# Kernel optimization log

Hardware: AMD Instinct MI355X
Metric: run time of the kernel (lower is better)

The kernel has to match this reference:

```python
import jax, jax.numpy as jnp
import numpy as np

H = 128  # LSTM hidden size


def lstm_layer(x, Wih, Whh, bih, bhh):
    # x: [B, T, Fin]; Wih: [4H, Fin]; Whh: [4H, H]; biases: [4H]
    xg = jnp.einsum('btf,gf->btg', x, Wih) + bih  # precompute input gates [B,T,4H]
    B = x.shape[0]
    h0 = jnp.zeros((B, H), x.dtype)
    c0 = jnp.zeros((B, H), x.dtype)

    def step(carry, xt):
        h, c = carry
        g = xt + h @ Whh.T + bhh  # [B,4H]
        i, f, gg, o = jnp.split(g, 4, axis=-1)  # torch gate order: i,f,g,o
        i = jax.nn.sigmoid(i)
        f = jax.nn.sigmoid(f)
        gg = jnp.tanh(gg)
        o = jax.nn.sigmoid(o)
        c = f * c + i * gg
        h = o * jnp.tanh(c)
        return (h, c), h

    (hT, cT), hs = jax.lax.scan(step, (h0, c0), jnp.swapaxes(xg, 0, 1))
    return jnp.swapaxes(hs, 0, 1), hT  # all-step outputs [B,T,H], final h [B,H]


def setup_inputs() -> dict:
    key = jax.random.key(0)
    ks = jax.random.split(key, 20)
    B, T, F = 512, 912, 32
    s = 1.0 / np.sqrt(H)  # torch LSTM/Linear init scale
    u = lambda k, shape: jax.random.uniform(k, shape, jnp.float32, -s, s)
    return {
        'x': jax.random.normal(ks[0], (B, T, F), jnp.float32),
        'Wih0': u(ks[1], (4 * H, F)),
        'Whh0': u(ks[2], (4 * H, H)),
        'bih0': u(ks[3], (4 * H,)),
        'bhh0': u(ks[4], (4 * H,)),
        'Wih123': u(ks[5], (3, 4 * H, H)),
        'Whh123': u(ks[6], (3, 4 * H, H)),
        'bih123': u(ks[7], (3, 4 * H)),
        'bhh123': u(ks[8], (3, 4 * H)),
        'Wopt': u(ks[9], (4, H)), 'bopt': u(ks[10], (4,)),
        'Wlot': u(ks[11], (4, H)), 'blot': u(ks[12], (4,)),
        'Wtp': u(ks[13], (4, H)), 'btp': u(ks[14], (4,)),
        'Wsl': u(ks[15], (4, H)), 'bsl': u(ks[16], (4,)),
    }


def reference(x, Wih0, Whh0, bih0, bhh0, Wih123, Whh123, bih123, bhh123,
              Wopt, bopt, Wlot, blot, Wtp, btp, Wsl, bsl):
    out, h0f = lstm_layer(x, Wih0, Whh0, bih0, bhh0)
    finals = [h0f]
    for l in range(3):  # fixed small layer loop
        out, hf = lstm_layer(out, Wih123[l], Whh123[l], bih123[l], bhh123[l])
        finals.append(hf)
    hN = jnp.stack(finals)  # h_n: [4, B, H] (final hidden per layer, as torch returns)
    # heads: Sequential applies softmax/sigmoid once, forward applies it again
    opt = jax.nn.softmax(jax.nn.softmax(hN @ Wopt.T + bopt, axis=-1), axis=-1)
    lot = jax.nn.sigmoid(jax.nn.sigmoid(hN @ Wlot.T + blot))
    tp = jax.nn.sigmoid(jax.nn.sigmoid(hN @ Wtp.T + btp))
    sl = jax.nn.sigmoid(jax.nn.sigmoid(hN @ Wsl.T + bsl))
    return (opt, tp, sl, lot)
```

## Files before the change

kernel.cpp:

```cpp
#include <hip/hip_runtime.h>

#define DEV __device__ __forceinline__

typedef __attribute__((ext_vector_type(8))) short short8;
typedef __attribute__((ext_vector_type(4))) float floatx4;
typedef unsigned long long ull;

static constexpr int B_ = 512, T_ = 912, H_ = 128, F_ = 32;
static constexpr size_t HN_OFF   = 1024;
static constexpr size_t XT_OFF   = HN_OFF + (size_t)4 * 512 * 128 * 2;
static constexpr size_t RING_OFF = XT_OFF + (size_t)T_ * B_ * F_ * 2;
static constexpr size_t RING_BPG = 8 * 32768;

template <int N> struct IC { static constexpr int value = N; };

DEV unsigned short bf16rne(float f) {
    unsigned u = __builtin_bit_cast(unsigned, f);
    u += 0x7FFFu + ((u >> 16) & 1u);
    return (unsigned short)(u >> 16);
}
DEV float bf16tof(unsigned short u) {
    return __builtin_bit_cast(float, ((unsigned)u) << 16);
}
DEV float fastsig(float y) {
    return __builtin_amdgcn_rcpf(1.f + __builtin_amdgcn_exp2f(y));
}
DEV float sigm(float x) { return fastsig(-1.44269504f * x); }
DEV unsigned ald(const unsigned* p) {
    return __hip_atomic_load(p, __ATOMIC_RELAXED, __HIP_MEMORY_SCOPE_AGENT);
}
DEV void ast32(unsigned* p, unsigned v) {
    __hip_atomic_store(p, v, __ATOMIC_RELAXED, __HIP_MEMORY_SCOPE_AGENT);
}
DEV ull ald8(const ull* p) {
    return __hip_atomic_load(p, __ATOMIC_RELAXED, __HIP_MEMORY_SCOPE_AGENT);
}
DEV void ast8(ull* p, ull v) {
    __hip_atomic_store(p, v, __ATOMIC_RELAXED, __HIP_MEMORY_SCOPE_AGENT);
}
DEV void bar_fast() {
    asm volatile("s_waitcnt lgkmcnt(0)\n\ts_barrier" ::: "memory");
}

__global__ __launch_bounds__(256) void xpose(const float* __restrict__ x,
                                             unsigned short* __restrict__ xT) {
    int tid = blockIdx.x * 256 + threadIdx.x;
    if (tid >= B_ * T_ * 4) return;
    int k = tid & 3;
    int r = tid >> 2;
    int b = r / T_;
    int t = r - b * T_;
    const float* p = x + ((size_t)r * 32 + k * 8);
    short8 v;
#pragma unroll
    for (int j = 0; j < 8; j++) v[j] = (short)bf16rne(p[j]);
    *(short8*)(xT + ((size_t)t * 512 + b) * 32 + k * 8) = v;
}

__global__ __launch_bounds__(512, 2) void lstm_scan(
    const float* __restrict__ Wih0, const float* __restrict__ Whh0,
    const float* __restrict__ bih0, const float* __restrict__ bhh0,
    const float* __restrict__ Wih123, const float* __restrict__ Whh123,
    const float* __restrict__ bih123, const float* __restrict__ bhh123,
    char* __restrict__ ws) {
    const int tid  = threadIdx.x;
    const int wv   = tid >> 6;
    const int lane = tid & 63;
    const int col  = lane & 15;
    const int quad = lane >> 4;
    const int layer = blockIdx.x >> 5;
    const int grp   = blockIdx.x & 31;
    const int b0    = grp * 16;

    unsigned* flags = (unsigned*)ws;
    unsigned* cons  = (unsigned*)(ws + 512);
    char* hN8 = ws + HN_OFF;
    const char* xTB = ws + XT_OFF;

    __shared__ unsigned short Ah[16][16][132];
    __shared__ unsigned short Xl[16][16][132];
    char* AhB = (char*)Ah;
    char* XlB = (char*)Xl;

    for (int i = tid; i < 16 * 16 * 132; i += 512) {
        ((unsigned short*)Ah)[i] = 0;
        ((unsigned short*)Xl)[i] = 0;
    }

    short8 wh[4][4];
    short8 wx[4][4];
    float  bias_q[4];
    {
        const float *Wih, *Whh, *bih, *bhh;
        int kin, KX;
        if (layer == 0) { Wih = Wih0; Whh = Whh0; bih = bih0; bhh = bhh0; kin = 32; KX = 1; }
        else {
            Wih = Wih123 + (size_t)(layer - 1) * 512 * 128;
            Whh = Whh123 + (size_t)(layer - 1) * 512 * 128;
            bih = bih123 + (size_t)(layer - 1) * 512;
            bhh = bhh123 + (size_t)(layer - 1) * 512;
            kin = 128; KX = 4;
        }
#pragma unroll
        for (int q = 0; q < 4; q++) {
            const float sc = (q == 2) ? -2.88539008f : -1.44269504f;
            int row = q * 128 + wv * 16 + col;
            bias_q[q] = (bih[row] + bhh[row]) * sc;
#pragma unroll
            for (int kt = 0; kt < 4; kt++) {
                const float* ph = Whh + (size_t)row * 128 + kt * 32 + quad * 8;
                short8 v;
#pragma unroll
                for (int j = 0; j < 8; j++) v[j] = (short)bf16rne(ph[j] * sc);
                wh[q][kt] = v;
            }
#pragma unroll
            for (int kt = 0; kt < 4; kt++) {
                short8 v = {0, 0, 0, 0, 0, 0, 0, 0};
                if (kt < KX) {
                    const float* px = Wih + (size_t)row * kin + kt * 32 + quad * 8;
#pragma unroll
                    for (int j = 0; j < 8; j++) v[j] = (short)bf16rne(px[j] * sc);
                }
                wx[q][kt] = v;
            }
        }
    }

    unsigned* myflag   = &flags[layer * 32 + grp];
    unsigned* prevflag = &flags[(layer > 0 ? layer - 1 : 0) * 32 + grp];
    unsigned* mycons   = &cons[(layer > 0 ? layer - 1 : 0) * 32 + grp];
    unsigned* nextcons = &cons[layer * 32 + grp];
    char* prodRing = ws + RING_OFF + (size_t)(layer * 32 + grp) * RING_BPG;
    char* consRing = ws + RING_OFF + (size_t)((layer > 0 ? layer - 1 : 0) * 32 + grp) * RING_BPG;

    const int ahrd  = col * 264 + quad * 16;
    const int hwr   = (quad * 4) * 264 + (wv * 16 + col) * 2;
    const int exOff = (tid >> 5) * 264 + (tid & 31) * 8;
    const int consOff = (tid >> 5) * 256 + (tid & 31) * 8;
    const int xgOff = (tid >> 6) * 32768 + b0 * 64 + (tid & 63) * 16;
    const int xlw0  = (tid >> 6) * 4224 + ((tid >> 2) & 15) * 264 + (tid & 3) * 16;

    ull    xin[8];
    short8 xv = {0, 0, 0, 0, 0, 0, 0, 0};
    unsigned pf = 0, pc = 0;
    float c4[4] = {0.f, 0.f, 0.f, 0.f};
    floatx4 accx[4];

    __syncthreads();

    if (layer > 0) {
        if (tid == 0) { while (ald(prevflag) < 2u) {} }
        __syncthreads();
#pragma unroll
        for (int j = 0; j < 16; j++) {
            ull d = ald8((const ull*)(consRing + (size_t)j * 4096 + consOff));
            *(ull*)(XlB + exOff + j * 4224) = d;
        }
    } else {
#pragma unroll
        for (int c0 = 0; c0 < 2; c0++) {
            short8 v = *(const short8*)(xTB + (size_t)c0 * 262144 + xgOff);
            *(short8*)(XlB + xlw0 + c0 * 33792) = v;
        }
    }
    __syncthreads();

    {
        short8 ax0[4];
#pragma unroll
        for (int kt = 0; kt < 4; kt++)
            ax0[kt] = *(const short8*)(XlB + ahrd + 0 * 4224 + kt * 64);
#pragma unroll
        for (int q = 0; q < 4; q++) {
            floatx4 a = {bias_q[q], bias_q[q], bias_q[q], bias_q[q]};
            accx[q] = a;
        }
#pragma unroll
        for (int kt = 0; kt < 4; kt++)
#pragma unroll
            for (int q = 0; q < 4; q++)
                accx[q] = __builtin_amdgcn_mfma_f32_16x16x32_bf16(ax0[kt], wx[q][kt], accx[q], 0, 0, 0);
    }

    int c = 0;
    auto step = [&](auto UC) {
        constexpr int u   = UC.value;
        constexpr bool bnd = (u == 0 || u == 8);
        constexpr bool stg = (u == 3 || u == 11);
        constexpr bool ver = (u == 7 || u == 15);
        constexpr int sph = (u < 8) ? 8 : 0;
        const int cc = c + (u >> 3);
        if (bnd) {
            if (tid == 0) {
                if (layer > 0 && cc <= 111) pf = ald(prevflag);
                if (layer < 3 && cc >= 8)   pc = ald(nextcons);
            }
            if (layer < 3 && cc >= 1) {
                char* rb = prodRing + (size_t)((cc - 1) & 7) * 32768 + tid * 8;
#pragma unroll
                for (int p = 0; p < 8; p++) {
                    ull hv = *(const ull*)(AhB + exOff + (sph + p) * 4224);
                    ast8((ull*)(rb + p * 4096), hv);
                }
            }
            if (layer > 0 && cc <= 112) {
                const char* rb2 = consRing + (size_t)((cc + 1) & 7) * 32768 + consOff;
#pragma unroll
                for (int j = 0; j < 8; j++)
                    xin[j] = ald8((const ull*)(rb2 + j * 4096));
            }
            if (layer == 0 && cc <= 112)
                xv = *(const short8*)(xTB + (size_t)(cc + 1) * 262144 + xgOff);
        }
        if (stg) {
            if (layer > 0) {
#pragma unroll
                for (int j = 0; j < 8; j++)
                    *(ull*)(XlB + exOff + (sph + j) * 4224) = xin[j];
            } else {
                *(short8*)(XlB + xlw0 + sph * 4224) = xv;
            }
        }
        short8 ah[4], axn[4];
#pragma unroll
        for (int kt = 0; kt < 4; kt++) {
            ah[kt]  = *(const short8*)(AhB + ahrd + ((u + 15) & 15) * 4224 + kt * 64);
            axn[kt] = *(const short8*)(XlB + ahrd + ((u + 1) & 15) * 4224 + kt * 64);
        }
        floatx4 acc[4];
#pragma unroll
        for (int q = 0; q < 4; q++) acc[q] = accx[q];
#pragma unroll
        for (int kt = 0; kt < 4; kt++)
#pragma unroll
            for (int q = 0; q < 4; q++)
                acc[q] = __builtin_amdgcn_mfma_f32_16x16x32_bf16(ah[kt], wh[q][kt], acc[q], 0, 0, 0);
#pragma unroll
        for (int q = 0; q < 4; q++) {
            floatx4 a = {bias_q[q], bias_q[q], bias_q[q], bias_q[q]};
            accx[q] = a;
        }
#pragma unroll
        for (int r = 0; r < 4; r++) {
            float iv = fastsig(acc[0][r]);
            float fv = fastsig(acc[1][r]);
            float gr = fastsig(acc[2][r]);
            float ov = fastsig(acc[3][r]);
#pragma unroll
            for (int q = 0; q < 4; q++)
                accx[q] = __builtin_amdgcn_mfma_f32_16x16x32_bf16(axn[r], wx[q][r], accx[q], 0, 0, 0);
            float gt = 2.f * gr - 1.f;
            float cv = fv * c4[r] + iv * gt;
            c4[r] = cv;
            float rc = fastsig(-2.88539008f * cv);
            float hv = ov * (2.f * rc - 1.f);
            *(unsigned short*)(AhB + hwr + u * 4224 + r * 264) = bf16rne(hv);
        }
        if (stg) {
            __syncthreads();
            if (tid == 0) {
                if (layer < 3 && cc >= 1) ast32(myflag, (unsigned)cc);
                if (layer > 0) ast32(mycons, (unsigned)(cc + 2));
            }
        } else {
            if (ver && tid == 0) {
                if (layer > 0 && cc <= 111) {
                    unsigned tgt = cc + 3;
                    if (pf < tgt) while (ald(prevflag) < tgt) {}
                }
                if (layer < 3 && cc >= 8) {
                    unsigned tgt = cc - 7;
                    if (pc < tgt) while (ald(nextcons) < tgt) {}
                }
            }
            bar_fast();
        }
    };

    for (c = 0; c < 114; c += 2) {
        step(IC<0>{});  step(IC<1>{});  step(IC<2>{});  step(IC<3>{});
        step(IC<4>{});  step(IC<5>{});  step(IC<6>{});  step(IC<7>{});
        step(IC<8>{});  step(IC<9>{});  step(IC<10>{}); step(IC<11>{});
        step(IC<12>{}); step(IC<13>{}); step(IC<14>{}); step(IC<15>{});
    }

    if (layer < 3) {
        char* rb = prodRing + (size_t)(113 & 7) * 32768 + tid * 8;
#pragma unroll
        for (int p = 0; p < 8; p++) {
            ull hv = *(const ull*)(AhB + exOff + (8 + p) * 4224);
            ast8((ull*)(rb + p * 4096), hv);
        }
    }
    __syncthreads();
    if (tid == 0 && layer < 3) ast32(myflag, 114u);
    {
        ull hv = *(const ull*)(AhB + exOff + 15 * 4224);
        *(ull*)(hN8 + ((size_t)layer * 512 + b0 + (tid >> 5)) * 256 + (tid & 31) * 8) = hv;
    }
}

__global__ __launch_bounds__(256) void heads(
    const unsigned short* __restrict__ hN,
    const float* __restrict__ Wopt, const float* __restrict__ bopt,
    const float* __restrict__ Wlot, const float* __restrict__ blot,
    const float* __restrict__ Wtp,  const float* __restrict__ btp,
    const float* __restrict__ Wsl,  const float* __restrict__ bsl,
    float* __restrict__ out) {
    int tid = blockIdx.x * 256 + threadIdx.x;
    if (tid >= 4 * 4 * 512) return;
    int b  = tid & 511;
    int l  = (tid >> 9) & 3;
    int hd = tid >> 11;
    const float *W, *bb;
    if      (hd == 0) { W = Wopt; bb = bopt; }
    else if (hd == 1) { W = Wtp;  bb = btp;  }
    else if (hd == 2) { W = Wsl;  bb = bsl;  }
    else              { W = Wlot; bb = blot; }
    const unsigned short* h = hN + ((size_t)l * 512 + b) * 128;
    float z0 = bb[0], z1 = bb[1], z2 = bb[2], z3 = bb[3];
    for (int i = 0; i < 128; i++) {
        float hv = bf16tof(h[i]);
        z0 += hv * W[0 * 128 + i];
        z1 += hv * W[1 * 128 + i];
        z2 += hv * W[2 * 128 + i];
        z3 += hv * W[3 * 128 + i];
    }
    float o0, o1, o2, o3;
    if (hd == 0) {
        float m = fmaxf(fmaxf(z0, z1), fmaxf(z2, z3));
        float e0 = __builtin_amdgcn_exp2f((z0 - m) * 1.44269504f);
        float e1 = __builtin_amdgcn_exp2f((z1 - m) * 1.44269504f);
        float e2 = __builtin_amdgcn_exp2f((z2 - m) * 1.44269504f);
        float e3 = __builtin_amdgcn_exp2f((z3 - m) * 1.44269504f);
        float rs = __builtin_amdgcn_rcpf(e0 + e1 + e2 + e3);
        float p0 = e0 * rs, p1 = e1 * rs, p2 = e2 * rs, p3 = e3 * rs;
        float m2 = fmaxf(fmaxf(p0, p1), fmaxf(p2, p3));
        float f0 = __builtin_amdgcn_exp2f((p0 - m2) * 1.44269504f);
        float f1 = __builtin_amdgcn_exp2f((p1 - m2) * 1.44269504f);
        float f2 = __builtin_amdgcn_exp2f((p2 - m2) * 1.44269504f);
        float f3 = __builtin_amdgcn_exp2f((p3 - m2) * 1.44269504f);
        float rs2 = __builtin_amdgcn_rcpf(f0 + f1 + f2 + f3);
        o0 = f0 * rs2; o1 = f1 * rs2; o2 = f2 * rs2; o3 = f3 * rs2;
    } else {
        o0 = sigm(sigm(z0)); o1 = sigm(sigm(z1));
        o2 = sigm(sigm(z2)); o3 = sigm(sigm(z3));
    }
    float* o = out + (size_t)hd * 8192 + ((size_t)l * 512 + b) * 4;
    o[0] = o0; o[1] = o1; o[2] = o2; o[3] = o3;
}

extern "C" void kernel_launch(void* const* d_in, const int* in_sizes, int n_in,
                              void* d_out, int out_size, void* d_ws, size_t ws_size,
                              hipStream_t stream) {
    (void)in_sizes; (void)n_in; (void)out_size; (void)ws_size;
    const float* x      = (const float*)d_in[0];
    const float* Wih0   = (const float*)d_in[1];
    const float* Whh0   = (const float*)d_in[2];
    const float* bih0   = (const float*)d_in[3];
    const float* bhh0   = (const float*)d_in[4];
    const float* Wih123 = (const float*)d_in[5];
    const float* Whh123 = (const float*)d_in[6];
    const float* bih123 = (const float*)d_in[7];
    const float* bhh123 = (const float*)d_in[8];
    const float* Wopt = (const float*)d_in[9];
    const float* bopt = (const float*)d_in[10];
    const float* Wlot = (const float*)d_in[11];
    const float* blot = (const float*)d_in[12];
    const float* Wtp  = (const float*)d_in[13];
    const float* btp  = (const float*)d_in[14];
    const float* Wsl  = (const float*)d_in[15];
    const float* bsl  = (const float*)d_in[16];
    char* ws = (char*)d_ws;

    hipMemsetAsync(ws, 0, 1024, stream);
    xpose<<<(B_ * T_ * 4 + 255) / 256, 256, 0, stream>>>(x, (unsigned short*)(ws + XT_OFF));
    lstm_scan<<<128, 512, 0, stream>>>(Wih0, Whh0, bih0, bhh0,
                                       Wih123, Whh123, bih123, bhh123, ws);
    heads<<<32, 256, 0, stream>>>((const unsigned short*)(ws + HN_OFF),
                                  Wopt, bopt, Wlot, blot, Wtp, btp, Wsl, bsl,
                                  (float*)d_out);
}
```

Measured before the change: 2.123 ms.

## Process 32 batch rows per block and feed input operands from registers

Each workgroup now handles 32 batch rows instead of 16, which halves the grid to 64 blocks and doubles the ring slot size. Every weight fragment held in registers is reused across two MFMA row tiles. The LDS staging buffer for inputs is removed: the next step's input fragments are loaded straight from the ring or the transposed x into registers, with the input-gate MFMAs issued each step before the recurrent ones. The aim is to amortise the per-step barrier and synchronisation cost over more work and to cut LDS traffic. The cost is a longer serial critical path per step and higher register pressure. The consumer acknowledgement offset also changes from cc+2 to cc.

```diff
diff --git a/kernel.cpp b/kernel.cpp
--- a/kernel.cpp
+++ b/kernel.cpp
@@ -5,12 +5,13 @@
 typedef __attribute__((ext_vector_type(8))) short short8;
 typedef __attribute__((ext_vector_type(4))) float floatx4;
 typedef unsigned long long ull;
+typedef __attribute__((ext_vector_type(2))) unsigned long long ull2;
 
 static constexpr int B_ = 512, T_ = 912, H_ = 128, F_ = 32;
 static constexpr size_t HN_OFF   = 1024;
 static constexpr size_t XT_OFF   = HN_OFF + (size_t)4 * 512 * 128 * 2;
 static constexpr size_t RING_OFF = XT_OFF + (size_t)T_ * B_ * F_ * 2;
-static constexpr size_t RING_BPG = 8 * 32768;
+static constexpr size_t RING_BPG = 8 * 65536;
 
 template <int N> struct IC { static constexpr int value = N; };
 
@@ -37,6 +38,12 @@
 }
 DEV void ast8(ull* p, ull v) {
     __hip_atomic_store(p, v, __ATOMIC_RELAXED, __HIP_MEMORY_SCOPE_AGENT);
+}
+DEV short8 ld_ring16(const char* p) {
+    ull2 r;
+    r.x = ald8((const ull*)p);
+    r.y = ald8((const ull*)(p + 8));
+    return __builtin_bit_cast(short8, r);
 }
 DEV void bar_fast() {
     asm volatile("s_waitcnt lgkmcnt(0)\n\ts_barrier" ::: "memory");
@@ -68,24 +75,20 @@
     const int lane = tid & 63;
     const int col  = lane & 15;
     const int quad = lane >> 4;
-    const int layer = blockIdx.x >> 5;
-    const int grp   = blockIdx.x & 31;
-    const int b0    = grp * 16;
+    const int layer = blockIdx.x >> 4;
+    const int grp   = blockIdx.x & 15;
+    const int b0    = grp * 32;
+    const bool lay0 = (layer == 0);
 
     unsigned* flags = (unsigned*)ws;
     unsigned* cons  = (unsigned*)(ws + 512);
     char* hN8 = ws + HN_OFF;
     const char* xTB = ws + XT_OFF;
 
-    __shared__ unsigned short Ah[16][16][132];
-    __shared__ unsigned short Xl[16][16][132];
+    __shared__ unsigned short Ah[16][32][132];
     char* AhB = (char*)Ah;
-    char* XlB = (char*)Xl;
-
-    for (int i = tid; i < 16 * 16 * 132; i += 512) {
-        ((unsigned short*)Ah)[i] = 0;
-        ((unsigned short*)Xl)[i] = 0;
-    }
+
+    for (int i = tid; i < 16 * 32 * 132; i += 512) ((unsigned short*)Ah)[i] = 0;
 
     short8 wh[4][4];
     short8 wx[4][4];
@@ -127,60 +130,42 @@
         }
     }
 
-    unsigned* myflag   = &flags[layer * 32 + grp];
-    unsigned* prevflag = &flags[(layer > 0 ? layer - 1 : 0) * 32 + grp];
-    unsigned* mycons   = &cons[(layer > 0 ? layer - 1 : 0) * 32 + grp];
-    unsigned* nextcons = &cons[layer * 32 + grp];
-    char* prodRing = ws + RING_OFF + (size_t)(layer * 32 + grp) * RING_BPG;
-    char* consRing = ws + RING_OFF + (size_t)((layer > 0 ? layer - 1 : 0) * 32 + grp) * RING_BPG;
+    unsigned* myflag   = &flags[layer * 16 + grp];
+    unsigned* prevflag = &flags[(layer > 0 ? layer - 1 : 0) * 16 + grp];
+    unsigned* mycons   = &cons[(layer > 0 ? layer - 1 : 0) * 16 + grp];
+    unsigned* nextcons = &cons[layer * 16 + grp];
+    char* prodRing = ws + RING_OFF + (size_t)(layer * 16 + grp) * RING_BPG;
+    char* consRing = ws + RING_OFF + (size_t)((layer > 0 ? layer - 1 : 0) * 16 + grp) * RING_BPG;
 
     const int ahrd  = col * 264 + quad * 16;
     const int hwr   = (quad * 4) * 264 + (wv * 16 + col) * 2;
-    const int exOff = (tid >> 5) * 264 + (tid & 31) * 8;
-    const int consOff = (tid >> 5) * 256 + (tid & 31) * 8;
-    const int xgOff = (tid >> 6) * 32768 + b0 * 64 + (tid & 63) * 16;
-    const int xlw0  = (tid >> 6) * 4224 + ((tid >> 2) & 15) * 264 + (tid & 3) * 16;
-
-    ull    xin[8];
-    short8 xv = {0, 0, 0, 0, 0, 0, 0, 0};
+    const int exRow = tid >> 4;
+    const int exB   = (tid & 15) * 16;
+    const int xroff = col * 256 + quad * 16;
+    const int xoff0 = (b0 + col) * 64 + quad * 16;
+
+    const short8 z8 = {0, 0, 0, 0, 0, 0, 0, 0};
+    short8 xb0[4], xb1[4];
+#pragma unroll
+    for (int kt = 0; kt < 4; kt++) { xb0[kt] = z8; xb1[kt] = z8; }
     unsigned pf = 0, pc = 0;
-    float c4[4] = {0.f, 0.f, 0.f, 0.f};
-    floatx4 accx[4];
+    float c8[8] = {0.f, 0.f, 0.f, 0.f, 0.f, 0.f, 0.f, 0.f};
 
     __syncthreads();
 
-    if (layer > 0) {
+    if (!lay0) {
         if (tid == 0) { while (ald(prevflag) < 2u) {} }
         __syncthreads();
-#pragma unroll
-        for (int j = 0; j < 16; j++) {
-            ull d = ald8((const ull*)(consRing + (size_t)j * 4096 + consOff));
-            *(ull*)(XlB + exOff + j * 4224) = d;
+        const char* rb0 = consRing + xroff;
+#pragma unroll
+        for (int kt = 0; kt < 4; kt++) {
+            xb0[kt] = ld_ring16(rb0 + kt * 64);
+            xb1[kt] = ld_ring16(rb0 + 4096 + kt * 64);
         }
     } else {
-#pragma unroll
-        for (int c0 = 0; c0 < 2; c0++) {
-            short8 v = *(const short8*)(xTB + (size_t)c0 * 262144 + xgOff);
-            *(short8*)(XlB + xlw0 + c0 * 33792) = v;
-        }
-    }
-    __syncthreads();
-
-    {
-        short8 ax0[4];
-#pragma unroll
-        for (int kt = 0; kt < 4; kt++)
-            ax0[kt] = *(const short8*)(XlB + ahrd + 0 * 4224 + kt * 64);
-#pragma unroll
-        for (int q = 0; q < 4; q++) {
-            floatx4 a = {bias_q[q], bias_q[q], bias_q[q], bias_q[q]};
-            accx[q] = a;
-        }
-#pragma unroll
-        for (int kt = 0; kt < 4; kt++)
-#pragma unroll
-            for (int q = 0; q < 4; q++)
-                accx[q] = __builtin_amdgcn_mfma_f32_16x16x32_bf16(ax0[kt], wx[q][kt], accx[q], 0, 0, 0);
+        const char* px = xTB + xoff0;
+        xb0[0] = *(const short8*)px;
+        xb1[0] = *(const short8*)(px + 1024);
     }
 
     int c = 0;
@@ -191,77 +176,104 @@
         constexpr bool ver = (u == 7 || u == 15);
         constexpr int sph = (u < 8) ? 8 : 0;
         const int cc = c + (u >> 3);
+        const int t  = cc * 8 + (u & 7);
+
         if (bnd) {
             if (tid == 0) {
                 if (layer > 0 && cc <= 111) pf = ald(prevflag);
                 if (layer < 3 && cc >= 8)   pc = ald(nextcons);
             }
             if (layer < 3 && cc >= 1) {
-                char* rb = prodRing + (size_t)((cc - 1) & 7) * 32768 + tid * 8;
+                char* rb = prodRing + (size_t)((cc - 1) & 7) * 65536 + exRow * 256 + exB;
+                const char* src = AhB + sph * 8448 + exRow * 264 + exB;
 #pragma unroll
                 for (int p = 0; p < 8; p++) {
-                    ull hv = *(const ull*)(AhB + exOff + (sph + p) * 4224);
-                    ast8((ull*)(rb + p * 4096), hv);
-                }
-            }
-            if (layer > 0 && cc <= 112) {
-                const char* rb2 = consRing + (size_t)((cc + 1) & 7) * 32768 + consOff;
-#pragma unroll
-                for (int j = 0; j < 8; j++)
-                    xin[j] = ald8((const ull*)(rb2 + j * 4096));
-            }
-            if (layer == 0 && cc <= 112)
-                xv = *(const short8*)(xTB + (size_t)(cc + 1) * 262144 + xgOff);
-        }
-        if (stg) {
-            if (layer > 0) {
-#pragma unroll
-                for (int j = 0; j < 8; j++)
-                    *(ull*)(XlB + exOff + (sph + j) * 4224) = xin[j];
-            } else {
-                *(short8*)(XlB + xlw0 + sph * 4224) = xv;
-            }
-        }
-        short8 ah[4], axn[4];
+                    ull h0 = *(const ull*)(src + p * 8448);
+                    ull h1 = *(const ull*)(src + p * 8448 + 8);
+                    ast8((ull*)(rb + p * 8192), h0);
+                    ast8((ull*)(rb + p * 8192 + 8), h1);
+                }
+            }
+        }
+
+        const int slR = (u + 15) & 15;
+        short8 ah0[4], ah1[4];
+        const char* ab = AhB + slR * 8448 + ahrd;
 #pragma unroll
         for (int kt = 0; kt < 4; kt++) {
-            ah[kt]  = *(const short8*)(AhB + ahrd + ((u + 15) & 15) * 4224 + kt * 64);
-            axn[kt] = *(const short8*)(XlB + ahrd + ((u + 1) & 15) * 4224 + kt * 64);
-        }
-        floatx4 acc[4];
-#pragma unroll
-        for (int q = 0; q < 4; q++) acc[q] = accx[q];
-#pragma unroll
-        for (int kt = 0; kt < 4; kt++)
-#pragma unroll
-            for (int q = 0; q < 4; q++)
-                acc[q] = __builtin_amdgcn_mfma_f32_16x16x32_bf16(ah[kt], wh[q][kt], acc[q], 0, 0, 0);
+            ah0[kt] = *(const short8*)(ab + kt * 64);
+            ah1[kt] = *(const short8*)(ab + 4224 + kt * 64);
+        }
+
+        floatx4 acc[4][2];
 #pragma unroll
         for (int q = 0; q < 4; q++) {
             floatx4 a = {bias_q[q], bias_q[q], bias_q[q], bias_q[q]};
-            accx[q] = a;
-        }
-#pragma unroll
-        for (int r = 0; r < 4; r++) {
-            float iv = fastsig(acc[0][r]);
-            float fv = fastsig(acc[1][r]);
-            float gr = fastsig(acc[2][r]);
-            float ov = fastsig(acc[3][r]);
-#pragma unroll
-            for (int q = 0; q < 4; q++)
-                accx[q] = __builtin_amdgcn_mfma_f32_16x16x32_bf16(axn[r], wx[q][r], accx[q], 0, 0, 0);
-            float gt = 2.f * gr - 1.f;
-            float cv = fv * c4[r] + iv * gt;
-            c4[r] = cv;
-            float rc = fastsig(-2.88539008f * cv);
-            float hv = ov * (2.f * rc - 1.f);
-            *(unsigned short*)(AhB + hwr + u * 4224 + r * 264) = bf16rne(hv);
-        }
+            acc[q][0] = a; acc[q][1] = a;
+        }
+        if (lay0) {
+#pragma unroll
+            for (int q = 0; q < 4; q++) {
+                acc[q][0] = __builtin_amdgcn_mfma_f32_16x16x32_bf16(xb0[0], wx[q][0], acc[q][0], 0, 0, 0);
+                acc[q][1] = __builtin_amdgcn_mfma_f32_16x16x32_bf16(xb1[0], wx[q][0], acc[q][1], 0, 0, 0);
+            }
+        } else {
+#pragma unroll
+            for (int kt = 0; kt < 4; kt++)
+#pragma unroll
+                for (int q = 0; q < 4; q++) {
+                    acc[q][0] = __builtin_amdgcn_mfma_f32_16x16x32_bf16(xb0[kt], wx[q][kt], acc[q][0], 0, 0, 0);
+                    acc[q][1] = __builtin_amdgcn_mfma_f32_16x16x32_bf16(xb1[kt], wx[q][kt], acc[q][1], 0, 0, 0);
+                }
+        }
+
+        if (t < 911) {
+            if (lay0) {
+                const char* px = xTB + (size_t)(t + 1) * 32768 + xoff0;
+                xb0[0] = *(const short8*)px;
+                xb1[0] = *(const short8*)(px + 1024);
+            } else {
+                const char* rb2 = consRing + (size_t)(((t + 1) >> 3) & 7) * 65536
+                                  + (size_t)((t + 1) & 7) * 8192 + xroff;
+#pragma unroll
+                for (int kt = 0; kt < 4; kt++) {
+                    xb0[kt] = ld_ring16(rb2 + kt * 64);
+                    xb1[kt] = ld_ring16(rb2 + 4096 + kt * 64);
+                }
+            }
+        }
+
+#pragma unroll
+        for (int kt = 0; kt < 4; kt++)
+#pragma unroll
+            for (int q = 0; q < 4; q++) {
+                acc[q][0] = __builtin_amdgcn_mfma_f32_16x16x32_bf16(ah0[kt], wh[q][kt], acc[q][0], 0, 0, 0);
+                acc[q][1] = __builtin_amdgcn_mfma_f32_16x16x32_bf16(ah1[kt], wh[q][kt], acc[q][1], 0, 0, 0);
+            }
+
+        char* hb = AhB + (u & 15) * 8448 + hwr;
+#pragma unroll
+        for (int rt = 0; rt < 2; rt++)
+#pragma unroll
+            for (int r = 0; r < 4; r++) {
+                float iv = fastsig(acc[0][rt][r]);
+                float fv = fastsig(acc[1][rt][r]);
+                float gr = fastsig(acc[2][rt][r]);
+                float ov = fastsig(acc[3][rt][r]);
+                float gt = 2.f * gr - 1.f;
+                const int ci = rt * 4 + r;
+                float cv = fv * c8[ci] + iv * gt;
+                c8[ci] = cv;
+                float rc = fastsig(-2.88539008f * cv);
+                float hv = ov * (2.f * rc - 1.f);
+                *(unsigned short*)(hb + rt * 4224 + r * 264) = bf16rne(hv);
+            }
+
         if (stg) {
             __syncthreads();
             if (tid == 0) {
                 if (layer < 3 && cc >= 1) ast32(myflag, (unsigned)cc);
-                if (layer > 0) ast32(mycons, (unsigned)(cc + 2));
+                if (layer > 0) ast32(mycons, (unsigned)cc);
             }
         } else {
             if (ver && tid == 0) {
@@ -286,18 +298,25 @@
     }
 
     if (layer < 3) {
-        char* rb = prodRing + (size_t)(113 & 7) * 32768 + tid * 8;
+        char* rb = prodRing + (size_t)(113 & 7) * 65536 + exRow * 256 + exB;
+        const char* src = AhB + 8 * 8448 + exRow * 264 + exB;
 #pragma unroll
         for (int p = 0; p < 8; p++) {
-            ull hv = *(const ull*)(AhB + exOff + (8 + p) * 4224);
-            ast8((ull*)(rb + p * 4096), hv);
+            ull h0 = *(const ull*)(src + p * 8448);
+            ull h1 = *(const ull*)(src + p * 8448 + 8);
+            ast8((ull*)(rb + p * 8192), h0);
+            ast8((ull*)(rb + p * 8192 + 8), h1);
         }
     }
     __syncthreads();
     if (tid == 0 && layer < 3) ast32(myflag, 114u);
     {
-        ull hv = *(const ull*)(AhB + exOff + 15 * 4224);
-        *(ull*)(hN8 + ((size_t)layer * 512 + b0 + (tid >> 5)) * 256 + (tid & 31) * 8) = hv;
+        const char* src = AhB + 15 * 8448 + exRow * 264 + exB;
+        ull h0 = *(const ull*)src;
+        ull h1 = *(const ull*)(src + 8);
+        char* dst = hN8 + ((size_t)layer * 512 + b0 + exRow) * 256 + exB;
+        *(ull*)dst = h0;
+        *(ull*)(dst + 8) = h1;
     }
 }
 
@@ -376,8 +395,8 @@
 
     hipMemsetAsync(ws, 0, 1024, stream);
     xpose<<<(B_ * T_ * 4 + 255) / 256, 256, 0, stream>>>(x, (unsigned short*)(ws + XT_OFF));
-    lstm_scan<<<128, 512, 0, stream>>>(Wih0, Whh0, bih0, bhh0,
-                                       Wih123, Whh123, bih123, bhh123, ws);
+    lstm_scan<<<64, 512, 0, stream>>>(Wih0, Whh0, bih0, bhh0,
+                                      Wih123, Whh123, bih123, bhh123, ws);
     heads<<<32, 256, 0, stream>>>((const unsigned short*)(ws + HN_OFF),
                                   Wopt, bopt, Wlot, blot, Wtp, btp, Wsl, bsl,
                                   (float*)d_out);
```

After: 5.116 ms. 2.41x slower.

## Process two 16-row batch groups per block to halve scan grid

Applied to the files above, without the earlier changes.

Each block now handles two independent 16-sequence groups (A and B), interleaving their recurrent MFMA chains, so the grid shrinks from 128 to 64 blocks. The input projection is computed inline each step (layer 0 reads x directly from global memory) instead of being pipelined one step ahead. The ring exchange is reworked into per-step slot stores and loads with an 8-step chunk. The aim is to hide MFMA and transcendental latency through two independent dependency chains per wave, and to cut the number of cross-block flag handoffs. The cost is twice the per-step work on each block's critical path, the input-GEMM latency now sitting on that path, and fewer CUs in use.

```diff
diff --git a/kernel.cpp b/kernel.cpp
--- a/kernel.cpp
+++ b/kernel.cpp
@@ -68,23 +68,28 @@
     const int lane = tid & 63;
     const int col  = lane & 15;
     const int quad = lane >> 4;
-    const int layer = blockIdx.x >> 5;
-    const int grp   = blockIdx.x & 31;
-    const int b0    = grp * 16;
+    const int layer = blockIdx.x >> 4;
+    const int g     = blockIdx.x & 15;
+    const int b0    = g * 32;
+    const bool lay0 = (layer == 0);
 
     unsigned* flags = (unsigned*)ws;
     unsigned* cons  = (unsigned*)(ws + 512);
     char* hN8 = ws + HN_OFF;
     const char* xTB = ws + XT_OFF;
 
-    __shared__ unsigned short Ah[16][16][132];
-    __shared__ unsigned short Xl[16][16][132];
-    char* AhB = (char*)Ah;
-    char* XlB = (char*)Xl;
-
-    for (int i = tid; i < 16 * 16 * 132; i += 512) {
-        ((unsigned short*)Ah)[i] = 0;
-        ((unsigned short*)Xl)[i] = 0;
+    __shared__ unsigned short AhA[8][16][132];
+    __shared__ unsigned short AhB[8][16][132];
+    __shared__ unsigned short XlA[8][16][132];
+    __shared__ unsigned short XlB[8][16][132];
+    char* AhAB = (char*)AhA;
+    char* AhBB = (char*)AhB;
+    char* XlAB = (char*)XlA;
+    char* XlBB = (char*)XlB;
+
+    for (int i = tid; i < 8 * 16 * 132; i += 512) {
+        ((unsigned short*)AhA)[i] = 0; ((unsigned short*)AhB)[i] = 0;
+        ((unsigned short*)XlA)[i] = 0; ((unsigned short*)XlB)[i] = 0;
     }
 
     short8 wh[4][4];
@@ -127,150 +132,192 @@
         }
     }
 
-    unsigned* myflag   = &flags[layer * 32 + grp];
-    unsigned* prevflag = &flags[(layer > 0 ? layer - 1 : 0) * 32 + grp];
-    unsigned* mycons   = &cons[(layer > 0 ? layer - 1 : 0) * 32 + grp];
-    unsigned* nextcons = &cons[layer * 32 + grp];
-    char* prodRing = ws + RING_OFF + (size_t)(layer * 32 + grp) * RING_BPG;
-    char* consRing = ws + RING_OFF + (size_t)((layer > 0 ? layer - 1 : 0) * 32 + grp) * RING_BPG;
+    unsigned* myflag   = &flags[layer * 16 + g];
+    unsigned* prevflag = &flags[(layer > 0 ? layer - 1 : 0) * 16 + g];
+    unsigned* mycons   = &cons[(layer > 0 ? layer - 1 : 0) * 16 + g];
+    unsigned* nextcons = &cons[layer * 16 + g];
+    char* prodA = ws + RING_OFF + (size_t)(layer * 32 + 2 * g) * RING_BPG;
+    char* prodB = prodA + RING_BPG;
+    char* consAp = ws + RING_OFF + (size_t)((layer > 0 ? layer - 1 : 0) * 32 + 2 * g) * RING_BPG;
+    char* consBp = consAp + RING_BPG;
 
     const int ahrd  = col * 264 + quad * 16;
     const int hwr   = (quad * 4) * 264 + (wv * 16 + col) * 2;
-    const int exOff = (tid >> 5) * 264 + (tid & 31) * 8;
-    const int consOff = (tid >> 5) * 256 + (tid & 31) * 8;
-    const int xgOff = (tid >> 6) * 32768 + b0 * 64 + (tid & 63) * 16;
-    const int xlw0  = (tid >> 6) * 4224 + ((tid >> 2) & 15) * 264 + (tid & 3) * 16;
-
-    ull    xin[8];
-    short8 xv = {0, 0, 0, 0, 0, 0, 0, 0};
+    const int exA   = (tid >> 5) * 264 + (tid & 31) * 8;
+    const int rgo   = tid << 3;
+    const int xoffA = (b0 + col) * 64 + quad * 16;
+
+    ull xrA[2] = {0, 0}, xrB[2] = {0, 0};
     unsigned pf = 0, pc = 0;
-    float c4[4] = {0.f, 0.f, 0.f, 0.f};
-    floatx4 accx[4];
+    float c4A[4] = {0.f, 0.f, 0.f, 0.f};
+    float c4B[4] = {0.f, 0.f, 0.f, 0.f};
 
     __syncthreads();
 
-    if (layer > 0) {
+    if (!lay0) {
         if (tid == 0) { while (ald(prevflag) < 2u) {} }
         __syncthreads();
 #pragma unroll
-        for (int j = 0; j < 16; j++) {
-            ull d = ald8((const ull*)(consRing + (size_t)j * 4096 + consOff));
-            *(ull*)(XlB + exOff + j * 4224) = d;
-        }
-    } else {
-#pragma unroll
-        for (int c0 = 0; c0 < 2; c0++) {
-            short8 v = *(const short8*)(xTB + (size_t)c0 * 262144 + xgOff);
-            *(short8*)(XlB + xlw0 + c0 * 33792) = v;
-        }
-    }
-    __syncthreads();
-
-    {
-        short8 ax0[4];
-#pragma unroll
-        for (int kt = 0; kt < 4; kt++)
-            ax0[kt] = *(const short8*)(XlB + ahrd + 0 * 4224 + kt * 64);
-#pragma unroll
-        for (int q = 0; q < 4; q++) {
-            floatx4 a = {bias_q[q], bias_q[q], bias_q[q], bias_q[q]};
-            accx[q] = a;
-        }
-#pragma unroll
-        for (int kt = 0; kt < 4; kt++)
-#pragma unroll
-            for (int q = 0; q < 4; q++)
-                accx[q] = __builtin_amdgcn_mfma_f32_16x16x32_bf16(ax0[kt], wx[q][kt], accx[q], 0, 0, 0);
+        for (int s = 0; s < 6; s++) {
+            ull a = ald8((const ull*)(consAp + s * 4096 + rgo));
+            ull b = ald8((const ull*)(consBp + s * 4096 + rgo));
+            *(ull*)(XlAB + s * 4224 + exA) = a;
+            *(ull*)(XlBB + s * 4224 + exA) = b;
+        }
+        xrA[0] = ald8((const ull*)(consAp + 6 * 4096 + rgo));
+        xrB[0] = ald8((const ull*)(consBp + 6 * 4096 + rgo));
+        xrA[1] = ald8((const ull*)(consAp + 7 * 4096 + rgo));
+        xrB[1] = ald8((const ull*)(consBp + 7 * 4096 + rgo));
+        __syncthreads();
     }
 
     int c = 0;
     auto step = [&](auto UC) {
         constexpr int u   = UC.value;
-        constexpr bool bnd = (u == 0 || u == 8);
-        constexpr bool stg = (u == 3 || u == 11);
-        constexpr bool ver = (u == 7 || u == 15);
-        constexpr int sph = (u < 8) ? 8 : 0;
-        const int cc = c + (u >> 3);
-        if (bnd) {
-            if (tid == 0) {
-                if (layer > 0 && cc <= 111) pf = ald(prevflag);
-                if (layer < 3 && cc >= 8)   pc = ald(nextcons);
-            }
-            if (layer < 3 && cc >= 1) {
-                char* rb = prodRing + (size_t)((cc - 1) & 7) * 32768 + tid * 8;
-#pragma unroll
-                for (int p = 0; p < 8; p++) {
-                    ull hv = *(const ull*)(AhB + exOff + (sph + p) * 4224);
-                    ast8((ull*)(rb + p * 4096), hv);
-                }
-            }
-            if (layer > 0 && cc <= 112) {
-                const char* rb2 = consRing + (size_t)((cc + 1) & 7) * 32768 + consOff;
-#pragma unroll
-                for (int j = 0; j < 8; j++)
-                    xin[j] = ald8((const ull*)(rb2 + j * 4096));
-            }
-            if (layer == 0 && cc <= 112)
-                xv = *(const short8*)(xTB + (size_t)(cc + 1) * 262144 + xgOff);
-        }
-        if (stg) {
-            if (layer > 0) {
-#pragma unroll
-                for (int j = 0; j < 8; j++)
-                    *(ull*)(XlB + exOff + (sph + j) * 4224) = xin[j];
-            } else {
-                *(short8*)(XlB + xlw0 + sph * 4224) = xv;
-            }
-        }
-        short8 ah[4], axn[4];
-#pragma unroll
-        for (int kt = 0; kt < 4; kt++) {
-            ah[kt]  = *(const short8*)(AhB + ahrd + ((u + 15) & 15) * 4224 + kt * 64);
-            axn[kt] = *(const short8*)(XlB + ahrd + ((u + 1) & 15) * 4224 + kt * 64);
-        }
-        floatx4 acc[4];
-#pragma unroll
-        for (int q = 0; q < 4; q++) acc[q] = accx[q];
-#pragma unroll
-        for (int kt = 0; kt < 4; kt++)
-#pragma unroll
-            for (int q = 0; q < 4; q++)
-                acc[q] = __builtin_amdgcn_mfma_f32_16x16x32_bf16(ah[kt], wh[q][kt], acc[q], 0, 0, 0);
+        constexpr int eSl = (u + 7) & 7;
+        constexpr int xSl = u;
+        constexpr int sSl = (u + 6) & 7;
+        constexpr int pp  = u & 1;
+        const int t = c * 8 + u;
+
+        if (u == 0 && tid == 0) {
+            if (layer > 0 && c <= 111) pf = ald(prevflag);
+            if (layer < 3 && c >= 8)   pc = ald(nextcons);
+        }
+
+        if (layer < 3 && t > 0) {
+            const int ch = ((u == 0) ? (c - 1) : c) & 7;
+            ull hA = *(const ull*)(AhAB + eSl * 4224 + exA);
+            ull hB = *(const ull*)(AhBB + eSl * 4224 + exA);
+            ast8((ull*)(prodA + (size_t)ch * 32768 + eSl * 4096 + rgo), hA);
+            ast8((ull*)(prodB + (size_t)ch * 32768 + eSl * 4096 + rgo), hB);
+        }
+
+        floatx4 accA[4];
 #pragma unroll
         for (int q = 0; q < 4; q++) {
             floatx4 a = {bias_q[q], bias_q[q], bias_q[q], bias_q[q]};
-            accx[q] = a;
-        }
-#pragma unroll
-        for (int r = 0; r < 4; r++) {
-            float iv = fastsig(acc[0][r]);
-            float fv = fastsig(acc[1][r]);
-            float gr = fastsig(acc[2][r]);
-            float ov = fastsig(acc[3][r]);
-#pragma unroll
-            for (int q = 0; q < 4; q++)
-                accx[q] = __builtin_amdgcn_mfma_f32_16x16x32_bf16(axn[r], wx[q][r], accx[q], 0, 0, 0);
-            float gt = 2.f * gr - 1.f;
-            float cv = fv * c4[r] + iv * gt;
-            c4[r] = cv;
-            float rc = fastsig(-2.88539008f * cv);
-            float hv = ov * (2.f * rc - 1.f);
-            *(unsigned short*)(AhB + hwr + u * 4224 + r * 264) = bf16rne(hv);
-        }
-        if (stg) {
+            accA[q] = a;
+        }
+        {
+            short8 ahA_[4];
+            const char* ab = AhAB + eSl * 4224 + ahrd;
+#pragma unroll
+            for (int kt = 0; kt < 4; kt++) ahA_[kt] = *(const short8*)(ab + kt * 64);
+            if (lay0) {
+                short8 ax = *(const short8*)(xTB + (size_t)t * 32768 + xoffA);
+#pragma unroll
+                for (int q = 0; q < 4; q++)
+                    accA[q] = __builtin_amdgcn_mfma_f32_16x16x32_bf16(ax, wx[q][0], accA[q], 0, 0, 0);
+            } else {
+                const char* xab = XlAB + xSl * 4224 + ahrd;
+#pragma unroll
+                for (int kt = 0; kt < 4; kt++) {
+                    short8 ax = *(const short8*)(xab + kt * 64);
+#pragma unroll
+                    for (int q = 0; q < 4; q++)
+                        accA[q] = __builtin_amdgcn_mfma_f32_16x16x32_bf16(ax, wx[q][kt], accA[q], 0, 0, 0);
+                }
+            }
+#pragma unroll
+            for (int kt = 0; kt < 4; kt++)
+#pragma unroll
+                for (int q = 0; q < 4; q++)
+                    accA[q] = __builtin_amdgcn_mfma_f32_16x16x32_bf16(ahA_[kt], wh[q][kt], accA[q], 0, 0, 0);
+        }
+
+        floatx4 accB[4];
+#pragma unroll
+        for (int q = 0; q < 4; q++) {
+            floatx4 a = {bias_q[q], bias_q[q], bias_q[q], bias_q[q]};
+            accB[q] = a;
+        }
+        {
+            short8 ahB_[4];
+            const char* ab = AhBB + eSl * 4224 + ahrd;
+#pragma unroll
+            for (int kt = 0; kt < 4; kt++) ahB_[kt] = *(const short8*)(ab + kt * 64);
+            if (lay0) {
+                short8 ax = *(const short8*)(xTB + (size_t)t * 32768 + xoffA + 1024);
+#pragma unroll
+                for (int q = 0; q < 4; q++)
+                    accB[q] = __builtin_amdgcn_mfma_f32_16x16x32_bf16(ax, wx[q][0], accB[q], 0, 0, 0);
+            } else {
+                const char* xab = XlBB + xSl * 4224 + ahrd;
+#pragma unroll
+                for (int kt = 0; kt < 4; kt++) {
+                    short8 ax = *(const short8*)(xab + kt * 64);
+#pragma unroll
+                    for (int q = 0; q < 4; q++)
+                        accB[q] = __builtin_amdgcn_mfma_f32_16x16x32_bf16(ax, wx[q][kt], accB[q], 0, 0, 0);
+                }
+            }
+#pragma unroll
+            for (int kt = 0; kt < 4; kt++)
+#pragma unroll
+                for (int q = 0; q < 4; q++)
+                    accB[q] = __builtin_amdgcn_mfma_f32_16x16x32_bf16(ahB_[kt], wh[q][kt], accB[q], 0, 0, 0);
+        }
+
+        if (!lay0) {
+            if (t + 6 <= 911) {
+                *(ull*)(XlAB + sSl * 4224 + exA) = xrA[pp];
+                *(ull*)(XlBB + sSl * 4224 + exA) = xrB[pp];
+            }
+            if (t <= 903) {
+                const int lch = (c + 1) & 7;
+                xrA[pp] = ald8((const ull*)(consAp + (size_t)lch * 32768 + xSl * 4096 + rgo));
+                xrB[pp] = ald8((const ull*)(consBp + (size_t)lch * 32768 + xSl * 4096 + rgo));
+            }
+        }
+
+        {
+            char* hb = AhAB + xSl * 4224 + hwr;
+#pragma unroll
+            for (int r = 0; r < 4; r++) {
+                float iv = fastsig(accA[0][r]);
+                float fv = fastsig(accA[1][r]);
+                float gr = fastsig(accA[2][r]);
+                float ov = fastsig(accA[3][r]);
+                float gt = 2.f * gr - 1.f;
+                float cv = fv * c4A[r] + iv * gt;
+                c4A[r] = cv;
+                float rc = fastsig(-2.88539008f * cv);
+                float hv = ov * (2.f * rc - 1.f);
+                *(unsigned short*)(hb + r * 264) = bf16rne(hv);
+            }
+        }
+        {
+            char* hb = AhBB + xSl * 4224 + hwr;
+#pragma unroll
+            for (int r = 0; r < 4; r++) {
+                float iv = fastsig(accB[0][r]);
+                float fv = fastsig(accB[1][r]);
+                float gr = fastsig(accB[2][r]);
+                float ov = fastsig(accB[3][r]);
+                float gt = 2.f * gr - 1.f;
+                float cv = fv * c4B[r] + iv * gt;
+                c4B[r] = cv;
+                float rc = fastsig(-2.88539008f * cv);
+                float hv = ov * (2.f * rc - 1.f);
+                *(unsigned short*)(hb + r * 264) = bf16rne(hv);
+            }
+        }
+
+        if constexpr (u == 3) {
             __syncthreads();
             if (tid == 0) {
-                if (layer < 3 && cc >= 1) ast32(myflag, (unsigned)cc);
-                if (layer > 0) ast32(mycons, (unsigned)(cc + 2));
+                if (layer < 3 && c >= 1) ast32(myflag, (unsigned)c);
+                if (layer > 0) ast32(mycons, (unsigned)c);
             }
         } else {
-            if (ver && tid == 0) {
-                if (layer > 0 && cc <= 111) {
-                    unsigned tgt = cc + 3;
+            if (u == 7 && tid == 0) {
+                if (layer > 0 && c <= 111) {
+                    unsigned tgt = c + 3;
                     if (pf < tgt) while (ald(prevflag) < tgt) {}
                 }
-                if (layer < 3 && cc >= 8) {
-                    unsigned tgt = cc - 7;
+                if (layer < 3 && c >= 8) {
+                    unsigned tgt = c - 7;
                     if (pc < tgt) while (ald(nextcons) < tgt) {}
                 }
             }
@@ -278,26 +325,25 @@
         }
     };
 
-    for (c = 0; c < 114; c += 2) {
-        step(IC<0>{});  step(IC<1>{});  step(IC<2>{});  step(IC<3>{});
-        step(IC<4>{});  step(IC<5>{});  step(IC<6>{});  step(IC<7>{});
-        step(IC<8>{});  step(IC<9>{});  step(IC<10>{}); step(IC<11>{});
-        step(IC<12>{}); step(IC<13>{}); step(IC<14>{}); step(IC<15>{});
+    for (c = 0; c < 114; ++c) {
+        step(IC<0>{}); step(IC<1>{}); step(IC<2>{}); step(IC<3>{});
+        step(IC<4>{}); step(IC<5>{}); step(IC<6>{}); step(IC<7>{});
     }
 
     if (layer < 3) {
-        char* rb = prodRing + (size_t)(113 & 7) * 32768 + tid * 8;
-#pragma unroll
-        for (int p = 0; p < 8; p++) {
-            ull hv = *(const ull*)(AhB + exOff + (8 + p) * 4224);
-            ast8((ull*)(rb + p * 4096), hv);
-        }
+        ull hA = *(const ull*)(AhAB + 7 * 4224 + exA);
+        ull hB = *(const ull*)(AhBB + 7 * 4224 + exA);
+        ast8((ull*)(prodA + (size_t)(113 & 7) * 32768 + 7 * 4096 + rgo), hA);
+        ast8((ull*)(prodB + (size_t)(113 & 7) * 32768 + 7 * 4096 + rgo), hB);
     }
     __syncthreads();
     if (tid == 0 && layer < 3) ast32(myflag, 114u);
     {
-        ull hv = *(const ull*)(AhB + exOff + 15 * 4224);
-        *(ull*)(hN8 + ((size_t)layer * 512 + b0 + (tid >> 5)) * 256 + (tid & 31) * 8) = hv;
+        ull hA = *(const ull*)(AhAB + 7 * 4224 + exA);
+        ull hB = *(const ull*)(AhBB + 7 * 4224 + exA);
+        char* dA = hN8 + ((size_t)layer * 512 + b0 + (tid >> 5)) * 256 + (tid & 31) * 8;
+        *(ull*)dA = hA;
+        *(ull*)(dA + 16 * 256) = hB;
     }
 }
 
@@ -376,8 +422,8 @@
 
     hipMemsetAsync(ws, 0, 1024, stream);
     xpose<<<(B_ * T_ * 4 + 255) / 256, 256, 0, stream>>>(x, (unsigned short*)(ws + XT_OFF));
-    lstm_scan<<<128, 512, 0, stream>>>(Wih0, Whh0, bih0, bhh0,
-                                       Wih123, Whh123, bih123, bhh123, ws);
+    lstm_scan<<<64, 512, 0, stream>>>(Wih0, Whh0, bih0, bhh0,
+                                      Wih123, Whh123, bih123, bhh123, ws);
     heads<<<32, 256, 0, stream>>>((const unsigned short*)(ws + HN_OFF),
                                   Wopt, bopt, Wlot, blot, Wtp, btp, Wsl, bsl,
                                   (float*)d_out);
```

Result: slower. 4.556 ms (+114.6%).

## Spread ring export per step and interleave gate sigmoids with MFMA chains

Applied to the files above, without the earlier changes.

Each step now exports the previous step's hidden state to the inter-layer ring, replacing the burst of eight exports at each 8-step boundary. The tail export is cut to the one remaining step to match. The recurrent MFMA loop is reordered per gate so each gate's sigmoid runs right after its chain, overlapping transcendental work with the other gates' MFMAs. The input-operand LDS loads are deferred to mid-chain to cut register pressure. The aim is to smooth memory traffic and shorten the serial critical path of each timestep, at the cost of more frequent small global stores.

```diff
diff --git a/kernel.cpp b/kernel.cpp
--- a/kernel.cpp
+++ b/kernel.cpp
@@ -191,19 +191,13 @@
         constexpr bool ver = (u == 7 || u == 15);
         constexpr int sph = (u < 8) ? 8 : 0;
         const int cc = c + (u >> 3);
+        const int t  = cc * 8 + (u & 7);
+
         if (bnd) {
             if (tid == 0) {
                 if (layer > 0 && cc <= 111) pf = ald(prevflag);
                 if (layer < 3 && cc >= 8)   pc = ald(nextcons);
             }
-            if (layer < 3 && cc >= 1) {
-                char* rb = prodRing + (size_t)((cc - 1) & 7) * 32768 + tid * 8;
-#pragma unroll
-                for (int p = 0; p < 8; p++) {
-                    ull hv = *(const ull*)(AhB + exOff + (sph + p) * 4224);
-                    ast8((ull*)(rb + p * 4096), hv);
-                }
-            }
             if (layer > 0 && cc <= 112) {
                 const char* rb2 = consRing + (size_t)((cc + 1) & 7) * 32768 + consOff;
 #pragma unroll
@@ -213,6 +207,14 @@
             if (layer == 0 && cc <= 112)
                 xv = *(const short8*)(xTB + (size_t)(cc + 1) * 262144 + xgOff);
         }
+
+        if (layer < 3 && t > 0) {
+            const int te = t - 1;
+            ull hv = *(const ull*)(AhB + exOff + ((u + 15) & 15) * 4224);
+            ast8((ull*)(prodRing + (size_t)((te >> 3) & 7) * 32768
+                        + (te & 7) * 4096 + tid * 8), hv);
+        }
+
         if (stg) {
             if (layer > 0) {
 #pragma unroll
@@ -222,20 +224,29 @@
                 *(short8*)(XlB + xlw0 + sph * 4224) = xv;
             }
         }
+
         short8 ah[4], axn[4];
 #pragma unroll
-        for (int kt = 0; kt < 4; kt++) {
-            ah[kt]  = *(const short8*)(AhB + ahrd + ((u + 15) & 15) * 4224 + kt * 64);
-            axn[kt] = *(const short8*)(XlB + ahrd + ((u + 1) & 15) * 4224 + kt * 64);
-        }
+        for (int kt = 0; kt < 4; kt++)
+            ah[kt] = *(const short8*)(AhB + ahrd + ((u + 15) & 15) * 4224 + kt * 64);
+
         floatx4 acc[4];
 #pragma unroll
-        for (int q = 0; q < 4; q++) acc[q] = accx[q];
-#pragma unroll
-        for (int kt = 0; kt < 4; kt++)
-#pragma unroll
-            for (int q = 0; q < 4; q++)
-                acc[q] = __builtin_amdgcn_mfma_f32_16x16x32_bf16(ah[kt], wh[q][kt], acc[q], 0, 0, 0);
+        for (int q = 0; q < 4; q++) {
+            floatx4 a = accx[q];
+#pragma unroll
+            for (int kt = 0; kt < 4; kt++)
+                a = __builtin_amdgcn_mfma_f32_16x16x32_bf16(ah[kt], wh[q][kt], a, 0, 0, 0);
+#pragma unroll
+            for (int r = 0; r < 4; r++) a[r] = fastsig(a[r]);
+            acc[q] = a;
+            if (q == 1) {
+#pragma unroll
+                for (int kt = 0; kt < 4; kt++)
+                    axn[kt] = *(const short8*)(XlB + ahrd + ((u + 1) & 15) * 4224 + kt * 64);
+            }
+        }
+
 #pragma unroll
         for (int q = 0; q < 4; q++) {
             floatx4 a = {bias_q[q], bias_q[q], bias_q[q], bias_q[q]};
@@ -243,10 +254,10 @@
         }
 #pragma unroll
         for (int r = 0; r < 4; r++) {
-            float iv = fastsig(acc[0][r]);
-            float fv = fastsig(acc[1][r]);
-            float gr = fastsig(acc[2][r]);
-            float ov = fastsig(acc[3][r]);
+            float iv = acc[0][r];
+            float fv = acc[1][r];
+            float gr = acc[2][r];
+            float ov = acc[3][r];
 #pragma unroll
             for (int q = 0; q < 4; q++)
                 accx[q] = __builtin_amdgcn_mfma_f32_16x16x32_bf16(axn[r], wx[q][r], accx[q], 0, 0, 0);
@@ -257,6 +268,7 @@
             float hv = ov * (2.f * rc - 1.f);
             *(unsigned short*)(AhB + hwr + u * 4224 + r * 264) = bf16rne(hv);
         }
+
         if (stg) {
             __syncthreads();
             if (tid == 0) {
@@ -286,12 +298,8 @@
     }
 
     if (layer < 3) {
-        char* rb = prodRing + (size_t)(113 & 7) * 32768 + tid * 8;
-#pragma unroll
-        for (int p = 0; p < 8; p++) {
-            ull hv = *(const ull*)(AhB + exOff + (8 + p) * 4224);
-            ast8((ull*)(rb + p * 4096), hv);
-        }
+        ull hv = *(const ull*)(AhB + exOff + 15 * 4224);
+        ast8((ull*)(prodRing + (size_t)(113 & 7) * 32768 + 7 * 4096 + tid * 8), hv);
     }
     __syncthreads();
     if (tid == 0 && layer < 3) ast32(myflag, 114u);
```

After: 2.155 ms. Within noise of the previous version (+1.5%).
